# Optimization experiments

Hardware: AMD Instinct MI355X
Metric: run time of the kernel (lower is better)

The kernel has to match this reference:

```python
import jax, jax.numpy as jnp
import numpy as np

B, C, H, W, K = 8, 256, 152, 152, 1024
MARGIN = 10.0
EPS = 1e-12  # F.normalize eps


def setup_inputs() -> dict:
    key = jax.random.key(0)
    k1, k2 = jax.random.split(key)
    output_id = jax.random.normal(k1, (B, C, H, W), dtype=jnp.float32)
    ind = jax.random.randint(k2, (B, K), 0, H * W)
    reg_mask = jnp.ones((B, K), dtype=jnp.int32)
    emb_scale = jnp.float32(10.0)
    return {"output_id": output_id, "ind": ind, "reg_mask": reg_mask, "emb_scale": emb_scale}


def reference(output_id, ind, reg_mask, emb_scale):
    b, c, h, w = output_id.shape
    # _tranpose_and_gather_feat: [B,C,H,W] -> [B,HW,C] -> gather ind -> [B,K,C]
    feat = output_id.transpose(0, 2, 3, 1).reshape(b, h * w, c)
    emb = jnp.take_along_axis(feat, ind[:, :, None], axis=1)  # [B,K,C]
    # emb_scale * F.normalize(emb)
    norm = jnp.maximum(jnp.linalg.norm(emb, axis=-1, keepdims=True), EPS)
    emb = emb_scale * (emb / norm)
    # pairwise euclidean distances per batch: [B,K,K]
    sq = jnp.sum(emb * emb, axis=-1)  # [B,K]
    d2 = sq[:, :, None] + sq[:, None, :] - 2.0 * jnp.einsum('bic,bjc->bij', emb, emb)
    dist = jnp.sqrt(jnp.maximum(d2, 0.0))
    # hardest negative: min over j != i, restricted to valid j
    valid = reg_mask > 0  # [B,K]
    big = jnp.float32(1e30)
    eye = jnp.eye(dist.shape[1], dtype=bool)[None]  # exclude self
    dist = jnp.where(eye | (~valid)[:, None, :], big, dist)
    neg_min = jnp.min(dist, axis=-1)  # [B,K]
    # HingeEmbeddingLoss with y = -1: mean over valid anchors of max(0, margin - d)
    hinge = jnp.maximum(MARGIN - neg_min, 0.0)
    vf = valid.astype(hinge.dtype)
    loss = jnp.sum(hinge * vf) / jnp.sum(vf)
    return loss
```

## Files before the change

kernel.cpp:

```cpp
#include <hip/hip_runtime.h>
#include <hip/hip_bf16.h>

#define Bz 8
#define Cc 256
#define HWp 23104
#define Kk 1024
#define BK (Bz*Kk)
#define MARGIN_F 10.0f
#define BIGF 1e30f
#define TILE 128
#define NBK 128

typedef __attribute__((ext_vector_type(8))) short bf16x8;
typedef __attribute__((ext_vector_type(4))) float f32x4;

__global__ __launch_bounds__(1024) void bucket_sort(
    const int* __restrict__ ind, uint* __restrict__ sorted,
    unsigned* __restrict__ neg, float* __restrict__ acc,
    unsigned* __restrict__ cnt)
{
    __shared__ uint cur[NBK], pre[NBK];
    const int b = blockIdx.x, tid = threadIdx.x;
    if (tid < NBK) cur[tid] = 0;
    neg[b * Kk + tid] = __float_as_uint(BIGF);
    if (b == 0 && tid < 2) acc[tid] = 0.f;
    if (b == 0 && tid == 0) *cnt = 0u;
    __syncthreads();
    int hw = ind[b * Kk + tid];
    int bk = hw >> 8;
    atomicAdd(&cur[bk], 1u);
    __syncthreads();
    uint mycount = (tid < NBK) ? cur[tid] : 0u;
    if (tid < NBK) pre[tid] = mycount;
    __syncthreads();
    #pragma unroll
    for (int off = 1; off < NBK; off <<= 1) {
        uint add = (tid < NBK && tid >= off) ? pre[tid - off] : 0u;
        __syncthreads();
        if (tid < NBK) pre[tid] += add;
        __syncthreads();
    }
    if (tid < NBK) cur[tid] = pre[tid] - mycount;
    __syncthreads();
    uint slot = atomicAdd(&cur[bk], 1u);
    sorted[b * Kk + slot] = ((uint)hw << 10) | (uint)tid;
}

__global__ __launch_bounds__(256) void sorted_gather(
    const float* __restrict__ x, const uint* __restrict__ sorted,
    __hip_bfloat16* __restrict__ embr, float* __restrict__ ssq_part)
{
    const int kq = blockIdx.x, cg = blockIdx.y, b = blockIdx.z;
    const int c0 = cg * 32;
    const int t = threadIdx.x;
    const int kl = t >> 2, cq = t & 3;
    uint e = sorted[b * Kk + kq * 64 + kl];
    int hw = (int)(e >> 10), k = (int)(e & 1023u);
    const float* xp = x + (size_t)(b * Cc + c0 + cq * 8) * HWp + hw;
    float v[8];
    #pragma unroll
    for (int j = 0; j < 8; ++j) v[j] = xp[(size_t)j * HWp];

    ushort ev[8]; float s2 = 0.f;
    #pragma unroll
    for (int j = 0; j < 8; ++j) {
        ev[j] = __hip_bfloat16_raw(__float2bfloat16(v[j])).x;
        float f = __uint_as_float((uint)ev[j] << 16);
        s2 += f * f;
    }
    s2 += __shfl_xor(s2, 1);
    s2 += __shfl_xor(s2, 2);

    uint4 o = make_uint4((uint)ev[0] | ((uint)ev[1] << 16),
                         (uint)ev[2] | ((uint)ev[3] << 16),
                         (uint)ev[4] | ((uint)ev[5] << 16),
                         (uint)ev[6] | ((uint)ev[7] << 16));
    *(uint4*)((ushort*)embr + (size_t)(b * Kk + k) * Cc + c0 + cq * 8) = o;
    if (cq == 0)
        ssq_part[cg * BK + b * Kk + k] = s2;
}

__global__ __launch_bounds__(256) void gram_mfma_min(
    const __hip_bfloat16* __restrict__ emb, const float* __restrict__ ssq_part,
    const int* __restrict__ mask, unsigned* __restrict__ neg)
{
    __shared__ __align__(16) short As[TILE * 64];
    __shared__ __align__(16) short Bs[TILE * 64];
    __shared__ float scl_i[TILE], scl_j[TILE];
    int b  = blockIdx.z;
    int i0 = blockIdx.y * TILE;
    int j0 = blockIdx.x * TILE;
    int tid = threadIdx.x;
    int w  = tid >> 6, l = tid & 63;
    int wr = w >> 1, wc = w & 1;
    int lr = l & 15, lg = l >> 4;

    {
        int m  = tid >> 7;
        int rl = tid & 127;
        int grow = b * Kk + (m ? j0 : i0) + rl;
        float s2 = 0.f;
        #pragma unroll
        for (int c = 0; c < 8; ++c) s2 += ssq_part[c * BK + grow];
        float sc = 10.0f / fmaxf(sqrtf(s2), 1e-12f);
        if (m) scl_j[rl] = sc; else scl_i[rl] = sc;
    }

    const short* E  = (const short*)emb + (size_t)b * Kk * Cc;
    const short* EA = E + (size_t)i0 * Cc;
    const short* EB = E + (size_t)j0 * Cc;

    const int lrow = l >> 3;
    const int lsub = (l & 7) ^ lrow;

    f32x4 acc[4][4] = {};
    for (int k0 = 0; k0 < Cc; k0 += 64) {
        #pragma unroll
        for (int q = 0; q < 4; ++q) {
            int t = w * 4 + q;
            int r = t * 8 + lrow;
            __builtin_amdgcn_global_load_lds(
                (const __attribute__((address_space(1))) void*)(EA + (size_t)r * Cc + k0 + lsub * 8),
                (__attribute__((address_space(3))) void*)&As[t * 512], 16, 0, 0);
            __builtin_amdgcn_global_load_lds(
                (const __attribute__((address_space(1))) void*)(EB + (size_t)r * Cc + k0 + lsub * 8),
                (__attribute__((address_space(3))) void*)&Bs[t * 512], 16, 0, 0);
        }
        __syncthreads();

        #pragma unroll
        for (int kk = 0; kk < 2; ++kk) {
            bf16x8 af[4], bf[4];
            #pragma unroll
            for (int f = 0; f < 4; ++f) {
                int ra = wr * 64 + f * 16 + lr;
                af[f] = *(const bf16x8*)&As[ra * 64 + (((kk * 4 + lg) ^ (ra & 7)) << 3)];
                int rb = wc * 64 + f * 16 + lr;
                bf[f] = *(const bf16x8*)&Bs[rb * 64 + (((kk * 4 + lg) ^ (rb & 7)) << 3)];
            }
            #pragma unroll
            for (int fi = 0; fi < 4; ++fi)
                #pragma unroll
                for (int fj = 0; fj < 4; ++fj)
                    acc[fi][fj] = __builtin_amdgcn_mfma_f32_16x16x32_bf16(
                                      af[fi], bf[fj], acc[fi][fj], 0, 0, 0);
        }
        __syncthreads();
    }

    const int* mb = mask + b * Kk;
    float cjv[4]; int jgv[4]; bool jva[4];
    #pragma unroll
    for (int fj = 0; fj < 4; ++fj) {
        int jl = wc * 64 + fj * 16 + lr;
        jgv[fj] = j0 + jl;
        cjv[fj] = scl_j[jl];
        jva[fj] = (mb[j0 + jl] != 0);
    }
    #pragma unroll
    for (int fi = 0; fi < 4; ++fi) {
        #pragma unroll
        for (int r = 0; r < 4; ++r) {
            int il = wr * 64 + fi * 16 + 4 * lg + r;
            int ig = i0 + il;
            float ci = scl_i[il];
            float m = BIGF;
            #pragma unroll
            for (int fj = 0; fj < 4; ++fj) {
                float d2 = fmaxf(200.0f - 2.0f * ci * cjv[fj] * acc[fi][fj][r], 0.0f);
                bool ok = jva[fj] && (jgv[fj] != ig);
                m = ok ? fminf(m, d2) : m;
            }
            #pragma unroll
            for (int off = 1; off < 16; off <<= 1)
                m = fminf(m, __shfl_xor(m, off));
            if (lr == 0)
                atomicMin(&neg[b * Kk + ig], __float_as_uint(m));
        }
    }
}

__global__ __launch_bounds__(256) void hinge_final(
    const unsigned* __restrict__ neg, const int* __restrict__ mask,
    float* __restrict__ acc, unsigned* __restrict__ cnt,
    float* __restrict__ out)
{
    const int tid = threadIdx.x;
    const int i = blockIdx.x * 256 + tid;
    float h = 0.f, v = 0.f;
    if (mask[i] != 0) {
        float d = sqrtf(__uint_as_float(neg[i]));
        h = fmaxf(MARGIN_F - d, 0.f);
        v = 1.f;
    }
    #pragma unroll
    for (int off = 32; off; off >>= 1) {
        h += __shfl_xor(h, off);
        v += __shfl_xor(v, off);
    }
    __shared__ float sh[4], sv[4];
    int w = tid >> 6;
    if ((tid & 63) == 0) { sh[w] = h; sv[w] = v; }
    __syncthreads();
    if (tid == 0) {
        atomicAdd(&acc[0], sh[0] + sh[1] + sh[2] + sh[3]);
        atomicAdd(&acc[1], sv[0] + sv[1] + sv[2] + sv[3]);
        unsigned prev = __hip_atomic_fetch_add(cnt, 1u, __ATOMIC_ACQ_REL,
                                               __HIP_MEMORY_SCOPE_AGENT);
        if (prev == 31u) {
            float H = atomicAdd(&acc[0], 0.0f);
            float V = atomicAdd(&acc[1], 0.0f);
            out[0] = H / V;
        }
    }
}

extern "C" void kernel_launch(void* const* d_in, const int* in_sizes, int n_in,
                              void* d_out, int out_size, void* d_ws, size_t ws_size,
                              hipStream_t stream) {
    const float* x    = (const float*)d_in[0];
    const int*   ind  = (const int*)d_in[1];
    const int*   mask = (const int*)d_in[2];
    float* out = (float*)d_out;

    __hip_bfloat16* embr = (__hip_bfloat16*)d_ws;
    float*    ssq_part = (float*)((char*)d_ws + (size_t)BK * Cc * sizeof(__hip_bfloat16));
    unsigned* neg    = (unsigned*)(ssq_part + 8 * BK);
    uint*     sorted = (uint*)(neg + BK);
    float*    acc    = (float*)(sorted + BK);
    unsigned* cnt    = (unsigned*)(acc + 2);

    bucket_sort<<<Bz, 1024, 0, stream>>>(ind, sorted, neg, acc, cnt);
    dim3 g1(16, Cc / 32, Bz);
    sorted_gather<<<g1, 256, 0, stream>>>(x, sorted, embr, ssq_part);
    dim3 g2(Kk / TILE, Kk / TILE, Bz);
    gram_mfma_min<<<g2, 256, 0, stream>>>(embr, ssq_part, mask, neg);
    hinge_final<<<32, 256, 0, stream>>>(neg, mask, acc, cnt, out);
}
```

Before: 49.23 us.

## Fuse bucket sort into gather via per-block spatial range filtering

Replaces the separate bucket_sort kernel and sorted_gather kernel with one filter_gather kernel. Each block owns a contiguous range of HW positions (RNG=1444, 16 ranges), scans all 1024 indices of its batch, keeps the ones in its range in a shared list, and gathers those channels. This drops a kernel launch and the global sorted buffer while keeping gather loads spatially local. The cost is that every block rereads the full index array and does shared atomics, and per-block work now varies with the index distribution.

```diff
diff --git a/kernel.cpp b/kernel.cpp
--- a/kernel.cpp
+++ b/kernel.cpp
@@ -4,80 +4,80 @@
 #define Bz 8
 #define Cc 256
 #define HWp 23104
+#define RNG 1444
 #define Kk 1024
 #define BK (Bz*Kk)
 #define MARGIN_F 10.0f
 #define BIGF 1e30f
 #define TILE 128
-#define NBK 128
 
 typedef __attribute__((ext_vector_type(8))) short bf16x8;
 typedef __attribute__((ext_vector_type(4))) float f32x4;
 
-__global__ __launch_bounds__(1024) void bucket_sort(
-    const int* __restrict__ ind, uint* __restrict__ sorted,
+__global__ __launch_bounds__(256) void filter_gather(
+    const float* __restrict__ x, const int* __restrict__ ind,
+    __hip_bfloat16* __restrict__ embr, float* __restrict__ ssq_part,
     unsigned* __restrict__ neg, float* __restrict__ acc,
     unsigned* __restrict__ cnt)
 {
-    __shared__ uint cur[NBK], pre[NBK];
-    const int b = blockIdx.x, tid = threadIdx.x;
-    if (tid < NBK) cur[tid] = 0;
-    neg[b * Kk + tid] = __float_as_uint(BIGF);
-    if (b == 0 && tid < 2) acc[tid] = 0.f;
-    if (b == 0 && tid == 0) *cnt = 0u;
+    __shared__ uint lst[Kk];
+    __shared__ uint lcnt;
+    const int rg = blockIdx.x, cg = blockIdx.y, b = blockIdx.z;
+    const int c0 = cg * 32;
+    const int t  = threadIdx.x;
+    const int lo = rg * RNG;
+
+    if (t == 0) lcnt = 0u;
+    if (rg == 0 && cg == 0) {
+        #pragma unroll
+        for (int q = 0; q < 4; ++q)
+            neg[b * Kk + q * 256 + t] = __float_as_uint(BIGF);
+        if (b == 0 && t < 2) acc[t] = 0.f;
+        if (b == 0 && t == 2) *cnt = 0u;
+    }
     __syncthreads();
-    int hw = ind[b * Kk + tid];
-    int bk = hw >> 8;
-    atomicAdd(&cur[bk], 1u);
+
+    const int* indb = ind + b * Kk;
+    #pragma unroll
+    for (int q = 0; q < 4; ++q) {
+        int k  = q * 256 + t;
+        int hw = indb[k];
+        unsigned off = (unsigned)(hw - lo);
+        if (off < (unsigned)RNG) {
+            uint slot = atomicAdd(&lcnt, 1u);
+            lst[slot] = ((uint)hw << 10) | (uint)k;
+        }
+    }
     __syncthreads();
-    uint mycount = (tid < NBK) ? cur[tid] : 0u;
-    if (tid < NBK) pre[tid] = mycount;
-    __syncthreads();
-    #pragma unroll
-    for (int off = 1; off < NBK; off <<= 1) {
-        uint add = (tid < NBK && tid >= off) ? pre[tid - off] : 0u;
-        __syncthreads();
-        if (tid < NBK) pre[tid] += add;
-        __syncthreads();
-    }
-    if (tid < NBK) cur[tid] = pre[tid] - mycount;
-    __syncthreads();
-    uint slot = atomicAdd(&cur[bk], 1u);
-    sorted[b * Kk + slot] = ((uint)hw << 10) | (uint)tid;
-}
-
-__global__ __launch_bounds__(256) void sorted_gather(
-    const float* __restrict__ x, const uint* __restrict__ sorted,
-    __hip_bfloat16* __restrict__ embr, float* __restrict__ ssq_part)
-{
-    const int kq = blockIdx.x, cg = blockIdx.y, b = blockIdx.z;
-    const int c0 = cg * 32;
-    const int t = threadIdx.x;
-    const int kl = t >> 2, cq = t & 3;
-    uint e = sorted[b * Kk + kq * 64 + kl];
-    int hw = (int)(e >> 10), k = (int)(e & 1023u);
-    const float* xp = x + (size_t)(b * Cc + c0 + cq * 8) * HWp + hw;
-    float v[8];
-    #pragma unroll
-    for (int j = 0; j < 8; ++j) v[j] = xp[(size_t)j * HWp];
-
-    ushort ev[8]; float s2 = 0.f;
-    #pragma unroll
-    for (int j = 0; j < 8; ++j) {
-        ev[j] = __hip_bfloat16_raw(__float2bfloat16(v[j])).x;
-        float f = __uint_as_float((uint)ev[j] << 16);
-        s2 += f * f;
-    }
-    s2 += __shfl_xor(s2, 1);
-    s2 += __shfl_xor(s2, 2);
-
-    uint4 o = make_uint4((uint)ev[0] | ((uint)ev[1] << 16),
-                         (uint)ev[2] | ((uint)ev[3] << 16),
-                         (uint)ev[4] | ((uint)ev[5] << 16),
-                         (uint)ev[6] | ((uint)ev[7] << 16));
-    *(uint4*)((ushort*)embr + (size_t)(b * Kk + k) * Cc + c0 + cq * 8) = o;
-    if (cq == 0)
-        ssq_part[cg * BK + b * Kk + k] = s2;
+    const int n = (int)lcnt;
+
+    const int cq = t & 3;
+    for (int e = t >> 2; e < n; e += 64) {
+        uint ent = lst[e];
+        int hw = (int)(ent >> 10), k = (int)(ent & 1023u);
+        const float* xp = x + (size_t)(b * Cc + c0 + cq * 8) * HWp + hw;
+        float v[8];
+        #pragma unroll
+        for (int j = 0; j < 8; ++j) v[j] = xp[(size_t)j * HWp];
+
+        ushort ev[8]; float s2 = 0.f;
+        #pragma unroll
+        for (int j = 0; j < 8; ++j) {
+            ev[j] = __hip_bfloat16_raw(__float2bfloat16(v[j])).x;
+            float f = __uint_as_float((uint)ev[j] << 16);
+            s2 += f * f;
+        }
+        s2 += __shfl_xor(s2, 1);
+        s2 += __shfl_xor(s2, 2);
+
+        uint4 o = make_uint4((uint)ev[0] | ((uint)ev[1] << 16),
+                             (uint)ev[2] | ((uint)ev[3] << 16),
+                             (uint)ev[4] | ((uint)ev[5] << 16),
+                             (uint)ev[6] | ((uint)ev[7] << 16));
+        *(uint4*)((ushort*)embr + (size_t)(b * Kk + k) * Cc + c0 + cq * 8) = o;
+        if (cq == 0)
+            ssq_part[cg * BK + b * Kk + k] = s2;
+    }
 }
 
 __global__ __launch_bounds__(256) void gram_mfma_min(
@@ -225,15 +225,13 @@
 
     __hip_bfloat16* embr = (__hip_bfloat16*)d_ws;
     float*    ssq_part = (float*)((char*)d_ws + (size_t)BK * Cc * sizeof(__hip_bfloat16));
-    unsigned* neg    = (unsigned*)(ssq_part + 8 * BK);
-    uint*     sorted = (uint*)(neg + BK);
-    float*    acc    = (float*)(sorted + BK);
-    unsigned* cnt    = (unsigned*)(acc + 2);
-
-    bucket_sort<<<Bz, 1024, 0, stream>>>(ind, sorted, neg, acc, cnt);
-    dim3 g1(16, Cc / 32, Bz);
-    sorted_gather<<<g1, 256, 0, stream>>>(x, sorted, embr, ssq_part);
-    dim3 g2(Kk / TILE, Kk / TILE, Bz);
-    gram_mfma_min<<<g2, 256, 0, stream>>>(embr, ssq_part, mask, neg);
+    unsigned* neg = (unsigned*)(ssq_part + 8 * BK);
+    float*    acc = (float*)(neg + BK);
+    unsigned* cnt = (unsigned*)(acc + 2);
+
+    dim3 g0(HWp / RNG, Cc / 32, Bz);
+    filter_gather<<<g0, 256, 0, stream>>>(x, ind, embr, ssq_part, neg, acc, cnt);
+    dim3 g1(Kk / TILE, Kk / TILE, Bz);
+    gram_mfma_min<<<g1, 256, 0, stream>>>(embr, ssq_part, mask, neg);
     hinge_final<<<32, 256, 0, stream>>>(neg, mask, acc, cnt, out);
 }
```

New measurement: 46.82 us (median of 2 runs). -4.9%, faster.
